# Optimization experiments

Hardware: AMD Instinct MI355X
Metric: run time of the kernel (lower is better)

## Reference

```python
import jax, jax.numpy as jnp
import numpy as np

D_MODEL = 512
N_LAYERS = 6
N_HEADS = 8
INNER = 2048
VOCAB = 2048
SEQ = 128
BATCH = 256
HEAD_DIM = D_MODEL // N_HEADS
EPS = 1e-5


def _pos_encoding(seq_len, d_model):
    pos = jnp.arange(seq_len, dtype=jnp.float32)[:, None]          # [S,1]
    i = jnp.arange(d_model // 2, dtype=jnp.float32)[None, :]       # [1,d/2]
    theta = pos / jnp.power(10000.0, 2.0 * i / d_model)            # [S,d/2]
    # interleave sin at even indices, cos at odd indices
    return jnp.stack([jnp.sin(theta), jnp.cos(theta)], axis=-1).reshape(seq_len, d_model)


def _layer_norm_2d(x):
    # F.layer_norm(x, (N, dims)): normalize over last TWO dims, no affine
    m = jnp.mean(x, axis=(1, 2), keepdims=True)
    v = jnp.mean(jnp.square(x - m), axis=(1, 2), keepdims=True)
    return (x - m) / jnp.sqrt(v + EPS)


def setup_inputs() -> dict:
    key = jax.random.key(0)
    ks = jax.random.split(key, 12)
    s = 0.02
    x = jax.random.randint(ks[0], (BATCH, SEQ), 0, VOCAB)
    emb = jax.random.normal(ks[1], (VOCAB, D_MODEL), jnp.float32) * s
    Wq = jax.random.normal(ks[2], (N_LAYERS, N_HEADS, D_MODEL, HEAD_DIM), jnp.float32) * s
    bq = jax.random.normal(ks[3], (N_LAYERS, N_HEADS, HEAD_DIM), jnp.float32) * s
    Wk = jax.random.normal(ks[4], (N_LAYERS, N_HEADS, D_MODEL, HEAD_DIM), jnp.float32) * s
    bk = jax.random.normal(ks[5], (N_LAYERS, N_HEADS, HEAD_DIM), jnp.float32) * s
    Wv = jax.random.normal(ks[6], (N_LAYERS, N_HEADS, D_MODEL, HEAD_DIM), jnp.float32) * s
    bv = jax.random.normal(ks[7], (N_LAYERS, N_HEADS, HEAD_DIM), jnp.float32) * s
    W1 = jax.random.normal(ks[8], (N_LAYERS, D_MODEL, INNER), jnp.float32) * s
    b1 = jax.random.normal(ks[9], (N_LAYERS, INNER), jnp.float32) * s
    W2 = jax.random.normal(ks[10], (N_LAYERS, INNER, D_MODEL), jnp.float32) * s
    b2 = jax.random.normal(ks[11], (N_LAYERS, D_MODEL), jnp.float32) * s
    return {"x": x, "emb": emb, "Wq": Wq, "bq": bq, "Wk": Wk, "bk": bk,
            "Wv": Wv, "bv": bv, "W1": W1, "b1": b1, "W2": W2, "b2": b2}


def reference(x, emb, Wq, bq, Wk, bk, Wv, bv, W1, b1, W2, b2):
    B, S = x.shape
    pe = _pos_encoding(SEQ, D_MODEL)
    h = emb[x] + pe[None, :, :]                                     # [B,S,D]
    scale = HEAD_DIM ** -0.5
    for l in range(N_LAYERS):
        q = jnp.einsum('bsd,hde->bhse', h, Wq[l]) + bq[l][None, :, None, :]
        k = jnp.einsum('bsd,hde->bhse', h, Wk[l]) + bk[l][None, :, None, :]
        v = jnp.einsum('bsd,hde->bhse', h, Wv[l]) + bv[l][None, :, None, :]
        scores = jnp.einsum('bhse,bhte->bhst', q, k) * scale        # no softmax!
        attn = jnp.einsum('bhst,bhte->bhse', scores, v)             # [B,H,S,E]
        attn = jnp.transpose(attn, (0, 2, 1, 3)).reshape(B, S, D_MODEL)
        h = _layer_norm_2d(h + attn)
        ff = jax.nn.relu(h @ W1[l] + b1[l]) @ W2[l] + b2[l]
        h = _layer_norm_2d(h + ff)
    return h
```

## Files before the change

kernel.cpp:

```cpp
#include <hip/hip_runtime.h>
#include <stdint.h>

#define NLAYERS 6
#define DMODEL  512
#define NHEADS  8
#define HDIM    64
#define INNER   2048
#define SEQ     128
#define BATCH   256
#define NTOK    (BATCH*SEQ)

typedef __attribute__((ext_vector_type(4))) float f32x4;
typedef __attribute__((ext_vector_type(8))) _Float16 hfrag;

typedef const __attribute__((address_space(1))) void* gas1p;
typedef __attribute__((address_space(3))) void* las3p;

__device__ __forceinline__ void load_lds16(const void* g, void* l) {
  __builtin_amdgcn_global_load_lds((gas1p)(uintptr_t)g, (las3p)(uint32_t)(uintptr_t)l, 16, 0, 0);
}

__device__ __forceinline__ ushort f2h(float f) {
  return __builtin_bit_cast(ushort, (_Float16)f);
}
__device__ __forceinline__ float h2f(ushort u) {
  return (float)__builtin_bit_cast(_Float16, u);
}

__device__ __forceinline__ f32x4 mfma16(hfrag a, hfrag b, f32x4 c) {
  return __builtin_amdgcn_mfma_f32_16x16x32_f16(a, b, c, 0, 0, 0);
}


__global__ void prep_qkv(const float* __restrict__ Wq, const float* __restrict__ Wk,
                         const float* __restrict__ Wv, const float* __restrict__ bq,
                         const float* __restrict__ bk, const float* __restrict__ bv,
                         ushort* __restrict__ Wt, float* __restrict__ biasq) {
  int idx = blockIdx.x*256 + threadIdx.x;
  if (idx >= NLAYERS*1536*512) return;
  const int k = idx & 511;
  const int n = (idx >> 9) % 1536;
  const int l = idx / (1536*512);
  const int which = n >> 9, hh = (n >> 6) & 7, e = n & 63;
  const float* W = (which == 0) ? Wq : ((which == 1) ? Wk : Wv);
  Wt[idx] = f2h(W[(((size_t)l*NHEADS + hh)*DMODEL + k)*HDIM + e]);
  if (k == 0) {
    const float* bb = (which == 0) ? bq : ((which == 1) ? bk : bv);
    biasq[l*1536 + n] = bb[((size_t)l*NHEADS + hh)*HDIM + e];
  }
}

__global__ void prep_w1(const float* __restrict__ W1, ushort* __restrict__ W1t) {
  int idx = blockIdx.x*256 + threadIdx.x;
  if (idx >= NLAYERS*INNER*512) return;
  const int k = idx & 511;
  const int n = (idx >> 9) % INNER;
  const int l = idx / (INNER*512);
  W1t[idx] = f2h(W1[((size_t)l*DMODEL + k)*INNER + n]);
}

__global__ void prep_w2(const float* __restrict__ W2, ushort* __restrict__ W2t) {
  int idx = blockIdx.x*256 + threadIdx.x;
  if (idx >= NLAYERS*512*INNER) return;
  const int k = idx & 2047;
  const int n = (idx >> 11) & 511;
  const int l = idx / (512*INNER);
  W2t[idx] = f2h(W2[((size_t)l*INNER + k)*DMODEL + n]);
}


__global__ void embed_kernel(const int* __restrict__ x, const float* __restrict__ emb,
                             ushort* __restrict__ hb) {
  const int t = blockIdx.x;
  const int i = threadIdx.x;
  const int s = t & (SEQ-1);
  const int tok = x[t];
  const float freq = expf(-(float)i * (9.210340371976184f / 256.0f));
  const float th = (float)s * freq;
  const float sn = sinf(th), cs = cosf(th);
  const size_t base = (size_t)t*DMODEL;
  const float v0 = emb[(size_t)tok*DMODEL + 2*i]     + sn;
  const float v1 = emb[(size_t)tok*DMODEL + 2*i + 1] + cs;
  *(uint*)(hb + base + 2*i) = (uint)f2h(v0) | ((uint)f2h(v1) << 16);
}


template<int K, int EPI>
__global__ __launch_bounds__(256, 2) void gemm_t(
    const ushort* __restrict__ A, const ushort* __restrict__ Bt,
    const float* __restrict__ bias, ushort* __restrict__ outb,
    const int ldc, const int nbn) {
  __shared__ __align__(16) char lds[73728];
  constexpr int NKT = K / 32;
  const int t = threadIdx.x;
  const int lane = t & 63, wc = t >> 6;
  const int cpx = (int)gridDim.x >> 3;
  const int wg  = ((int)blockIdx.x & 7) * cpx + ((int)blockIdx.x >> 3);
  const int bm = wg / nbn, bn = wg % nbn;

  const int fr = lane & 15;
  const int cxor = (((lane >> 4) ^ ((fr >> 1) & 3)) << 4);

  float bias_r[4];
  #pragma unroll
  for (int n = 0; n < 4; ++n) bias_r[n] = bias[bn*256 + wc*64 + n*16 + fr];
  asm volatile("" : "+v"(bias_r[0]), "+v"(bias_r[1]), "+v"(bias_r[2]), "+v"(bias_r[3]));

  const int srow = t >> 2;
  const int scc  = (t & 3) ^ ((t >> 3) & 3);
  const ushort* aSrc = A  + ((size_t)bm*128 + srow)*K + scc*8;
  const ushort* bSrc = Bt + ((size_t)bn*256 + srow)*K + scc*8;

  auto stage_t = [&](int j, int slot) {
    char* dst = lds + slot*24576 + t*16;
    const ushort* as = aSrc + j*32;
    load_lds16(as,                  dst);
    load_lds16(as + (size_t)64*K,   dst + 4096);
    const ushort* bs = bSrc + j*32;
    #pragma unroll
    for (int i = 0; i < 4; ++i)
      load_lds16(bs + (size_t)(i*64)*K, dst + 8192 + i*4096);
  };

  f32x4 acc[8][4] = {};

  stage_t(0, 0); stage_t(1, 1);
  asm volatile("s_waitcnt vmcnt(6)" ::: "memory");
  __builtin_amdgcn_s_barrier();

  int rs = 0, ss = 2;
  #pragma unroll 1
  for (int kt = 0; kt < NKT; ++kt) {
    const char* sl = lds + rs*24576;
    hfrag a[8], b[4];
    #pragma unroll
    for (int m = 0; m < 8; ++m)
      a[m] = *(const hfrag*)(sl + (m*16 + fr)*64 + cxor);
    #pragma unroll
    for (int n = 0; n < 4; ++n)
      b[n] = *(const hfrag*)(sl + 8192 + (wc*64 + n*16 + fr)*64 + cxor);
    if (kt + 2 < NKT) stage_t(kt + 2, ss);
    __builtin_amdgcn_s_setprio(1);
    #pragma unroll
    for (int m = 0; m < 8; ++m)
      #pragma unroll
      for (int n = 0; n < 4; ++n)
        acc[m][n] = mfma16(a[m], b[n], acc[m][n]);
    __builtin_amdgcn_s_setprio(0);
    if (kt + 2 < NKT) {
      asm volatile("s_waitcnt vmcnt(6)" ::: "memory");
    } else if (kt + 2 == NKT) {
      asm volatile("s_waitcnt vmcnt(0)" ::: "memory");
    }
    if (kt + 1 < NKT) __builtin_amdgcn_s_barrier();
    rs = (rs == 2) ? 0 : rs + 1;
    ss = (ss == 2) ? 0 : ss + 1;
  }

  #pragma unroll
  for (int m = 0; m < 8; ++m) {
    __syncthreads();
    #pragma unroll
    for (int n = 0; n < 4; ++n) {
      const int cc16 = wc*4 + n;
      #pragma unroll
      for (int r4 = 0; r4 < 4; ++r4) {
        const int row = ((lane >> 4) << 2) + r4;
        float v = acc[m][n][r4] + bias_r[n];
        if constexpr (EPI == 1) v = fmaxf(v, 0.0f);
        *(ushort*)(lds + row*512 + ((cc16 ^ (row >> 2)) << 5) + fr*2) = f2h(v);
      }
    }
    __syncthreads();
    const int er = t >> 4;
    ushort* gp = outb + (size_t)(bm*128 + m*16 + er)*ldc + bn*256;
    #pragma unroll
    for (int p = 0; p < 2; ++p) {
      const int cj = (t & 15) + p*16;
      const uint4 v = *(const uint4*)(lds + er*512 + (((cj >> 1) ^ (er >> 2)) << 5) + ((cj & 1) << 4));
      *(uint4*)(gp + cj*8) = v;
    }
  }
}


__global__ __launch_bounds__(256) void attn_kernel(
    const ushort* __restrict__ qkv, ushort* __restrict__ outb) {
  __shared__ __align__(16) ushort wbuf[4][8192];
  const int tid = threadIdx.x;
  const int w = tid >> 6, lane = tid & 63;
  const int bh = blockIdx.x*4 + w;
  const int b = bh >> 3, h = bh & 7;
  const ushort* tokbase = qkv + (size_t)b*SEQ*1536;
  ushort* lds = &wbuf[w][0];
  ushort* kch = lds;
  ushort* vch = lds + 2048;

  f32x4 acc1[4][4] = {};
  #pragma unroll 1
  for (int sb = 0; sb < 4; ++sb) {
    const int s0 = sb*32;
    const int sr = lane >> 1;
    #pragma unroll
    for (int i = 0; i < 4; ++i) {
      const int cc  = i*2 + (lane & 1);
      const int ccs = cc ^ (sr & 7);
      const ushort* g = tokbase + (size_t)(s0+sr)*1536 + h*64 + cc*8;
      *(uint4*)(kch + sr*64 + ccs*8) = *(const uint4*)(g + 512);
      *(uint4*)(vch + sr*64 + ccs*8) = *(const uint4*)(g + 1024);
    }
    hfrag ak[4], av[4];
    #pragma unroll
    for (int m = 0; m < 4; ++m) {
      const int e1 = m*16 + (lane & 15);
      const int ccb = e1 >> 3, el = e1 & 7;
      #pragma unroll
      for (int j = 0; j < 8; ++j) {
        const int s = (lane >> 4)*8 + j;
        ak[m][j] = __builtin_bit_cast(_Float16, kch[s*64 + ((ccb ^ (s & 7))*8) + el]);
        av[m][j] = __builtin_bit_cast(_Float16, vch[s*64 + ((ccb ^ (s & 7))*8) + el]);
      }
    }
    #pragma unroll
    for (int m = 0; m < 4; ++m)
      #pragma unroll
      for (int n = 0; n < 4; ++n)
        acc1[m][n] = mfma16(ak[m], av[n], acc1[m][n]);
  }

  ushort* tv = lds;
  #pragma unroll
  for (int m = 0; m < 4; ++m)
    #pragma unroll
    for (int n = 0; n < 4; ++n)
      #pragma unroll
      for (int r4 = 0; r4 < 4; ++r4) {
        const int e1 = m*16 + (lane >> 4)*4 + r4;
        const int e2 = n*16 + (lane & 15);
        tv[e2*72 + e1] = f2h(acc1[m][n][r4] * 0.125f);
      }

  f32x4 acc2[8][4] = {};
  #pragma unroll
  for (int eb = 0; eb < 2; ++eb) {
    const int e1b = eb*32 + (lane >> 4)*8;
    hfrag aq[8], bk2[4];
    #pragma unroll
    for (int m = 0; m < 8; ++m) {
      const int s = m*16 + (lane & 15);
      aq[m] = *(const hfrag*)(tokbase + (size_t)s*1536 + h*64 + e1b);
    }
    #pragma unroll
    for (int n = 0; n < 4; ++n) {
      const int e2 = n*16 + (lane & 15);
      bk2[n] = *(const hfrag*)(tv + e2*72 + e1b);
    }
    #pragma unroll
    for (int m = 0; m < 8; ++m)
      #pragma unroll
      for (int n = 0; n < 4; ++n)
        acc2[m][n] = mfma16(aq[m], bk2[n], acc2[m][n]);
  }

  const int fr = lane & 15;
  char* sb8 = (char*)lds;
  #pragma unroll
  for (int m = 0; m < 8; ++m)
    #pragma unroll
    for (int n = 0; n < 4; ++n)
      #pragma unroll
      for (int r4 = 0; r4 < 4; ++r4) {
        const int s = m*16 + ((lane >> 4) << 2) + r4;
        *(ushort*)(sb8 + s*128 + ((n ^ ((s >> 2) & 3)) << 5) + fr*2) = f2h(acc2[m][n][r4]);
      }
  ushort* ob = outb + ((size_t)b*SEQ)*DMODEL + h*64;
  #pragma unroll
  for (int rr = 0; rr < 16; ++rr) {
    const int r = rr*8 + (lane >> 3);
    const int cj = lane & 7;
    const uint4 v = *(const uint4*)(sb8 + r*128 + (((cj >> 1) ^ ((r >> 2) & 3)) << 5) + ((cj & 1) << 4));
    *(uint4*)(ob + (size_t)r*DMODEL + cj*8) = v;
  }
}


template<bool FINAL>
__global__ __launch_bounds__(1024) void resid_ln(
    const ushort* __restrict__ delta, ushort* __restrict__ hb, float* __restrict__ hf) {
  const int b = blockIdx.x;
  const size_t base = (size_t)b * (SEQ*DMODEL);
  uint4 cache[8];
  float s = 0.f, q = 0.f;
  #pragma unroll
  for (int j = 0; j < 8; ++j) {
    const size_t idx = base + (size_t)j*8192 + threadIdx.x*8;
    const uint4 hv = *(const uint4*)(hb + idx);
    const uint4 dv = *(const uint4*)(delta + idx);
    uint4 cv;
    #pragma unroll
    for (int c = 0; c < 4; ++c) {
      const uint hu = (&hv.x)[c], du = (&dv.x)[c];
      const float v0 = h2f((ushort)(hu & 0xffffu)) + h2f((ushort)(du & 0xffffu));
      const float v1 = h2f((ushort)(hu >> 16))     + h2f((ushort)(du >> 16));
      s += v0 + v1; q += v0*v0 + v1*v1;
      (&cv.x)[c] = (uint)f2h(v0) | ((uint)f2h(v1) << 16);
    }
    cache[j] = cv;
  }
  #pragma unroll
  for (int off = 32; off > 0; off >>= 1) {
    s += __shfl_down(s, off);
    q += __shfl_down(q, off);
  }
  __shared__ float ws_[16], wq_[16];
  __shared__ float stat[2];
  const int w = threadIdx.x >> 6, lane = threadIdx.x & 63;
  if (lane == 0) { ws_[w] = s; wq_[w] = q; }
  __syncthreads();
  if (threadIdx.x == 0) {
    float S = 0.f, Q = 0.f;
    #pragma unroll
    for (int i2 = 0; i2 < 16; ++i2) { S += ws_[i2]; Q += wq_[i2]; }
    const float mean = S * (1.0f/65536.0f);
    const float var  = Q * (1.0f/65536.0f) - mean*mean;
    stat[0] = mean; stat[1] = rsqrtf(var + 1e-5f);
  }
  __syncthreads();
  const float mean = stat[0], rstd = stat[1];
  #pragma unroll
  for (int j = 0; j < 8; ++j) {
    const size_t idx = base + (size_t)j*8192 + threadIdx.x*8;
    const uint4 cv = cache[j];
    if constexpr (FINAL) {
      #pragma unroll
      for (int c = 0; c < 4; ++c) {
        const uint u = (&cv.x)[c];
        const float o0 = (h2f((ushort)(u & 0xffffu)) - mean) * rstd;
        const float o1 = (h2f((ushort)(u >> 16))     - mean) * rstd;
        *(float2*)(hf + idx + c*2) = make_float2(o0, o1);
      }
    } else {
      uint4 ov;
      #pragma unroll
      for (int c = 0; c < 4; ++c) {
        const uint u = (&cv.x)[c];
        const float o0 = (h2f((ushort)(u & 0xffffu)) - mean) * rstd;
        const float o1 = (h2f((ushort)(u >> 16))     - mean) * rstd;
        (&ov.x)[c] = (uint)f2h(o0) | ((uint)f2h(o1) << 16);
      }
      *(uint4*)(hb + idx) = ov;
    }
  }
}


extern "C" void kernel_launch(void* const* d_in, const int* in_sizes, int n_in,
                              void* d_out, int out_size, void* d_ws, size_t ws_size,
                              hipStream_t stream) {
  const int*   x   = (const int*)d_in[0];
  const float* emb = (const float*)d_in[1];
  const float* Wq  = (const float*)d_in[2];
  const float* bq  = (const float*)d_in[3];
  const float* Wk  = (const float*)d_in[4];
  const float* bk  = (const float*)d_in[5];
  const float* Wv  = (const float*)d_in[6];
  const float* bv  = (const float*)d_in[7];
  const float* W1  = (const float*)d_in[8];
  const float* b1  = (const float*)d_in[9];
  const float* W2  = (const float*)d_in[10];
  const float* b2  = (const float*)d_in[11];
  float* h = (float*)d_out;

  char* p = (char*)d_ws;
  size_t off = 0;
  auto alloc = [&](size_t bytes) { char* r = p + off; off += (bytes + 255) & ~(size_t)255; return r; };
  ushort* Wqkv_t = (ushort*)alloc((size_t)NLAYERS*1536*512*2);
  ushort* W1t    = (ushort*)alloc((size_t)NLAYERS*INNER*512*2);
  ushort* W2t    = (ushort*)alloc((size_t)NLAYERS*512*INNER*2);
  float*  biasq  = (float*)alloc((size_t)NLAYERS*1536*4);
  ushort* hbf    = (ushort*)alloc((size_t)NTOK*512*2);
  ushort* big    = (ushort*)alloc((size_t)NTOK*2048*2);
  ushort* attnb  = (ushort*)alloc((size_t)NTOK*512*2);

  prep_qkv<<<(NLAYERS*1536*512 + 255)/256, 256, 0, stream>>>(Wq, Wk, Wv, bq, bk, bv, Wqkv_t, biasq);
  prep_w1<<<(NLAYERS*INNER*512 + 255)/256, 256, 0, stream>>>(W1, W1t);
  prep_w2<<<(NLAYERS*512*INNER + 255)/256, 256, 0, stream>>>(W2, W2t);
  embed_kernel<<<NTOK, 256, 0, stream>>>(x, emb, hbf);

  for (int l = 0; l < NLAYERS; ++l) {
    gemm_t<512,0><<<1536, 256, 0, stream>>>(
        hbf, Wqkv_t + (size_t)l*1536*512, biasq + (size_t)l*1536, big, 1536, 6);
    attn_kernel<<<BATCH*NHEADS/4, 256, 0, stream>>>(big, attnb);
    resid_ln<false><<<BATCH, 1024, 0, stream>>>(attnb, hbf, nullptr);
    gemm_t<512,1><<<2048, 256, 0, stream>>>(
        hbf, W1t + (size_t)l*INNER*512, b1 + (size_t)l*INNER, big, 2048, 8);
    gemm_t<2048,0><<<512, 256, 0, stream>>>(
        big, W2t + (size_t)l*512*INNER, b2 + (size_t)l*512, attnb, 512, 2);
    if (l == NLAYERS-1) {
      resid_ln<true><<<BATCH, 1024, 0, stream>>>(attnb, hbf, h);
    } else {
      resid_ln<false><<<BATCH, 1024, 0, stream>>>(attnb, hbf, nullptr);
    }
  }
}
```

Measured before the change: 1.750 ms.

## Enlarge GEMM tile to 256x256 with 8 waves and split-phase staging

New measurement: 1.764 ms. About the same (+0.8%).

```diff
diff --git a/kernel.cpp b/kernel.cpp
--- a/kernel.cpp
+++ b/kernel.cpp
@@ -86,14 +86,15 @@
 
 
 template<int K, int EPI>
-__global__ __launch_bounds__(256, 2) void gemm_t(
+__global__ __launch_bounds__(512, 2) void gemm_p(
     const ushort* __restrict__ A, const ushort* __restrict__ Bt,
     const float* __restrict__ bias, ushort* __restrict__ outb,
     const int ldc, const int nbn) {
-  __shared__ __align__(16) char lds[73728];
+  __shared__ __align__(16) char lds[98304];
   constexpr int NKT = K / 32;
   const int t = threadIdx.x;
-  const int lane = t & 63, wc = t >> 6;
+  const int lane = t & 63, w = t >> 6;
+  const int wr = w >> 2, wcn = w & 3;
   const int cpx = (int)gridDim.x >> 3;
   const int wg  = ((int)blockIdx.x & 7) * cpx + ((int)blockIdx.x >> 3);
   const int bm = wg / nbn, bn = wg % nbn;
@@ -103,52 +104,69 @@
 
   float bias_r[4];
   #pragma unroll
-  for (int n = 0; n < 4; ++n) bias_r[n] = bias[bn*256 + wc*64 + n*16 + fr];
+  for (int n = 0; n < 4; ++n) bias_r[n] = bias[bn*256 + wcn*64 + n*16 + fr];
   asm volatile("" : "+v"(bias_r[0]), "+v"(bias_r[1]), "+v"(bias_r[2]), "+v"(bias_r[3]));
 
   const int srow = t >> 2;
   const int scc  = (t & 3) ^ ((t >> 3) & 3);
-  const ushort* aSrc = A  + ((size_t)bm*128 + srow)*K + scc*8;
+  const ushort* aSrc = A  + ((size_t)bm*256 + srow)*K + scc*8;
   const ushort* bSrc = Bt + ((size_t)bn*256 + srow)*K + scc*8;
 
-  auto stage_t = [&](int j, int slot) {
-    char* dst = lds + slot*24576 + t*16;
+  auto stageA = [&](int j, int slot) {
+    char* dst = lds + slot*32768 + t*16;
     const ushort* as = aSrc + j*32;
-    load_lds16(as,                  dst);
-    load_lds16(as + (size_t)64*K,   dst + 4096);
+    load_lds16(as,                 dst);
+    load_lds16(as + (size_t)128*K, dst + 8192);
+  };
+  auto stageB = [&](int j, int slot) {
+    char* dst = lds + slot*32768 + 16384 + t*16;
     const ushort* bs = bSrc + j*32;
-    #pragma unroll
-    for (int i = 0; i < 4; ++i)
-      load_lds16(bs + (size_t)(i*64)*K, dst + 8192 + i*4096);
+    load_lds16(bs,                 dst);
+    load_lds16(bs + (size_t)128*K, dst + 8192);
   };
 
   f32x4 acc[8][4] = {};
 
-  stage_t(0, 0); stage_t(1, 1);
-  asm volatile("s_waitcnt vmcnt(6)" ::: "memory");
+  stageA(0, 0); stageB(0, 0); stageA(1, 1); stageB(1, 1);
+  asm volatile("s_waitcnt vmcnt(4)" ::: "memory");
   __builtin_amdgcn_s_barrier();
 
   int rs = 0, ss = 2;
   #pragma unroll 1
   for (int kt = 0; kt < NKT; ++kt) {
-    const char* sl = lds + rs*24576;
-    hfrag a[8], b[4];
-    #pragma unroll
-    for (int m = 0; m < 8; ++m)
-      a[m] = *(const hfrag*)(sl + (m*16 + fr)*64 + cxor);
+    const char* sl = lds + rs*32768;
+    hfrag a0[4], b0[4];
+    #pragma unroll
+    for (int m = 0; m < 4; ++m)
+      a0[m] = *(const hfrag*)(sl + (wr*128 + m*16 + fr)*64 + cxor);
     #pragma unroll
     for (int n = 0; n < 4; ++n)
-      b[n] = *(const hfrag*)(sl + 8192 + (wc*64 + n*16 + fr)*64 + cxor);
-    if (kt + 2 < NKT) stage_t(kt + 2, ss);
+      b0[n] = *(const hfrag*)(sl + 16384 + (wcn*64 + n*16 + fr)*64 + cxor);
+    if (kt + 2 < NKT) stageA(kt + 2, ss);
+    __builtin_amdgcn_s_barrier();
     __builtin_amdgcn_s_setprio(1);
     #pragma unroll
-    for (int m = 0; m < 8; ++m)
+    for (int m = 0; m < 4; ++m)
       #pragma unroll
       for (int n = 0; n < 4; ++n)
-        acc[m][n] = mfma16(a[m], b[n], acc[m][n]);
+        acc[m][n] = mfma16(a0[m], b0[n], acc[m][n]);
+    __builtin_amdgcn_s_setprio(0);
+    __builtin_amdgcn_s_barrier();
+    hfrag a1[4];
+    #pragma unroll
+    for (int m = 0; m < 4; ++m)
+      a1[m] = *(const hfrag*)(sl + (wr*128 + (m+4)*16 + fr)*64 + cxor);
+    if (kt + 2 < NKT) stageB(kt + 2, ss);
+    __builtin_amdgcn_s_barrier();
+    __builtin_amdgcn_s_setprio(1);
+    #pragma unroll
+    for (int m = 0; m < 4; ++m)
+      #pragma unroll
+      for (int n = 0; n < 4; ++n)
+        acc[m+4][n] = mfma16(a1[m], b0[n], acc[m+4][n]);
     __builtin_amdgcn_s_setprio(0);
     if (kt + 2 < NKT) {
-      asm volatile("s_waitcnt vmcnt(6)" ::: "memory");
+      asm volatile("s_waitcnt vmcnt(4)" ::: "memory");
     } else if (kt + 2 == NKT) {
       asm volatile("s_waitcnt vmcnt(0)" ::: "memory");
     }
@@ -162,22 +180,24 @@
     __syncthreads();
     #pragma unroll
     for (int n = 0; n < 4; ++n) {
-      const int cc16 = wc*4 + n;
       #pragma unroll
       for (int r4 = 0; r4 < 4; ++r4) {
-        const int row = ((lane >> 4) << 2) + r4;
+        const int sr32 = wr*16 + ((lane >> 4) << 2) + r4;
+        const int cc   = wcn*8 + n*2 + (fr >> 3);
+        const int ccs  = cc ^ (((sr32 >> 2) ^ sr32) & 3);
         float v = acc[m][n][r4] + bias_r[n];
         if constexpr (EPI == 1) v = fmaxf(v, 0.0f);
-        *(ushort*)(lds + row*512 + ((cc16 ^ (row >> 2)) << 5) + fr*2) = f2h(v);
+        *(ushort*)(lds + sr32*512 + ccs*16 + (fr & 7)*2) = f2h(v);
       }
     }
     __syncthreads();
-    const int er = t >> 4;
-    ushort* gp = outb + (size_t)(bm*128 + m*16 + er)*ldc + bn*256;
+    const int lr = t >> 4;
+    const int grow = bm*256 + (lr >> 4)*128 + m*16 + (lr & 15);
+    ushort* gp = outb + (size_t)grow*ldc + bn*256;
     #pragma unroll
     for (int p = 0; p < 2; ++p) {
       const int cj = (t & 15) + p*16;
-      const uint4 v = *(const uint4*)(lds + er*512 + (((cj >> 1) ^ (er >> 2)) << 5) + ((cj & 1) << 4));
+      const uint4 v = *(const uint4*)(lds + lr*512 + (cj ^ (((lr >> 2) ^ lr) & 3))*16);
       *(uint4*)(gp + cj*8) = v;
     }
   }
@@ -388,13 +408,13 @@
   embed_kernel<<<NTOK, 256, 0, stream>>>(x, emb, hbf);
 
   for (int l = 0; l < NLAYERS; ++l) {
-    gemm_t<512,0><<<1536, 256, 0, stream>>>(
+    gemm_p<512,0><<<768, 512, 0, stream>>>(
         hbf, Wqkv_t + (size_t)l*1536*512, biasq + (size_t)l*1536, big, 1536, 6);
     attn_kernel<<<BATCH*NHEADS/4, 256, 0, stream>>>(big, attnb);
     resid_ln<false><<<BATCH, 1024, 0, stream>>>(attnb, hbf, nullptr);
-    gemm_t<512,1><<<2048, 256, 0, stream>>>(
+    gemm_p<512,1><<<1024, 512, 0, stream>>>(
         hbf, W1t + (size_t)l*INNER*512, b1 + (size_t)l*INNER, big, 2048, 8);
-    gemm_t<2048,0><<<512, 256, 0, stream>>>(
+    gemm_p<2048,0><<<256, 512, 0, stream>>>(
         big, W2t + (size_t)l*512*INNER, b2 + (size_t)l*512, attnb, 512, 2);
     if (l == NLAYERS-1) {
       resid_ln<true><<<BATCH, 1024, 0, stream>>>(attnb, hbf, h);
```

## Rewrite GEMM with 256x256 tiles, 32x32 MFMA and double-buffered K=64 stages

Applied to the files above, without the earlier changes.

Result: slower. 2.180 ms (+24.5%).

```diff
diff --git a/kernel.cpp b/kernel.cpp
--- a/kernel.cpp
+++ b/kernel.cpp
@@ -10,8 +10,9 @@
 #define BATCH   256
 #define NTOK    (BATCH*SEQ)
 
-typedef __attribute__((ext_vector_type(4))) float f32x4;
-typedef __attribute__((ext_vector_type(8))) _Float16 hfrag;
+typedef __attribute__((ext_vector_type(4)))  float f32x4;
+typedef __attribute__((ext_vector_type(16))) float f32x16;
+typedef __attribute__((ext_vector_type(8)))  _Float16 hfrag;
 
 typedef const __attribute__((address_space(1))) void* gas1p;
 typedef __attribute__((address_space(3))) void* las3p;
@@ -29,6 +30,9 @@
 
 __device__ __forceinline__ f32x4 mfma16(hfrag a, hfrag b, f32x4 c) {
   return __builtin_amdgcn_mfma_f32_16x16x32_f16(a, b, c, 0, 0, 0);
+}
+__device__ __forceinline__ f32x16 mfma32(hfrag a, hfrag b, f32x16 c) {
+  return __builtin_amdgcn_mfma_f32_32x32x16_f16(a, b, c, 0, 0, 0);
 }
 
 
@@ -86,100 +90,92 @@
 
 
 template<int K, int EPI>
-__global__ __launch_bounds__(256, 2) void gemm_t(
+__global__ __launch_bounds__(256, 1) void gemm_w(
     const ushort* __restrict__ A, const ushort* __restrict__ Bt,
     const float* __restrict__ bias, ushort* __restrict__ outb,
     const int ldc, const int nbn) {
-  __shared__ __align__(16) char lds[73728];
-  constexpr int NKT = K / 32;
+  __shared__ __align__(16) char lds[131072];
+  constexpr int NKT = K / 64;
   const int t = threadIdx.x;
-  const int lane = t & 63, wc = t >> 6;
+  const int lane = t & 63, w = t >> 6;
+  const int wr = w >> 1, wc = w & 1;
   const int cpx = (int)gridDim.x >> 3;
   const int wg  = ((int)blockIdx.x & 7) * cpx + ((int)blockIdx.x >> 3);
   const int bm = wg / nbn, bn = wg % nbn;
 
-  const int fr = lane & 15;
-  const int cxor = (((lane >> 4) ^ ((fr >> 1) & 3)) << 4);
-
   float bias_r[4];
   #pragma unroll
-  for (int n = 0; n < 4; ++n) bias_r[n] = bias[bn*256 + wc*64 + n*16 + fr];
+  for (int n = 0; n < 4; ++n) bias_r[n] = bias[bn*256 + wc*128 + n*32 + (lane & 31)];
   asm volatile("" : "+v"(bias_r[0]), "+v"(bias_r[1]), "+v"(bias_r[2]), "+v"(bias_r[3]));
 
-  const int srow = t >> 2;
-  const int scc  = (t & 3) ^ ((t >> 3) & 3);
-  const ushort* aSrc = A  + ((size_t)bm*128 + srow)*K + scc*8;
-  const ushort* bSrc = Bt + ((size_t)bn*256 + srow)*K + scc*8;
-
-  auto stage_t = [&](int j, int slot) {
-    char* dst = lds + slot*24576 + t*16;
-    const ushort* as = aSrc + j*32;
-    load_lds16(as,                  dst);
-    load_lds16(as + (size_t)64*K,   dst + 4096);
-    const ushort* bs = bSrc + j*32;
-    #pragma unroll
-    for (int i = 0; i < 4; ++i)
-      load_lds16(bs + (size_t)(i*64)*K, dst + 8192 + i*4096);
+  const int srow = t >> 3;
+  const int gcc  = (t & 7) ^ (srow & 7);
+  const ushort* aSrc = A  + ((size_t)bm*256 + srow)*K + gcc*8;
+  const ushort* bSrc = Bt + ((size_t)bn*256 + srow)*K + gcc*8;
+
+  auto stage = [&](int j, int slot) {
+    char* da = lds + slot*65536 + t*16;
+    const ushort* as = aSrc + j*64;
+    const ushort* bs = bSrc + j*64;
+    #pragma unroll
+    for (int i = 0; i < 8; ++i) {
+      load_lds16(as + (size_t)(i*32)*K, da + i*4096);
+      load_lds16(bs + (size_t)(i*32)*K, da + 32768 + i*4096);
+    }
   };
 
-  f32x4 acc[8][4] = {};
-
-  stage_t(0, 0); stage_t(1, 1);
-  asm volatile("s_waitcnt vmcnt(6)" ::: "memory");
+  f32x16 acc[4][4] = {};
+
+  stage(0, 0);
+  asm volatile("s_waitcnt vmcnt(0)" ::: "memory");
   __builtin_amdgcn_s_barrier();
 
-  int rs = 0, ss = 2;
   #pragma unroll 1
   for (int kt = 0; kt < NKT; ++kt) {
-    const char* sl = lds + rs*24576;
-    hfrag a[8], b[4];
-    #pragma unroll
-    for (int m = 0; m < 8; ++m)
-      a[m] = *(const hfrag*)(sl + (m*16 + fr)*64 + cxor);
+    if (kt + 1 < NKT) stage(kt + 1, (kt + 1) & 1);
+    const char* sl = lds + (kt & 1)*65536;
+    const char* sa = sl + (size_t)(wr*128 + (lane & 31))*128;
+    const char* sb = sl + 32768 + (size_t)(wc*128 + (lane & 31))*128;
+    #pragma unroll
+    for (int kk = 0; kk < 4; ++kk) {
+      const int slotx = ((kk*2 + (lane >> 5)) ^ (lane & 7)) * 16;
+      hfrag a[4], b[4];
+      #pragma unroll
+      for (int m = 0; m < 4; ++m) a[m] = *(const hfrag*)(sa + m*4096 + slotx);
+      #pragma unroll
+      for (int n = 0; n < 4; ++n) b[n] = *(const hfrag*)(sb + n*4096 + slotx);
+      #pragma unroll
+      for (int m = 0; m < 4; ++m)
+        #pragma unroll
+        for (int n = 0; n < 4; ++n)
+          acc[m][n] = mfma32(a[m], b[n], acc[m][n]);
+    }
+    if (kt + 1 < NKT) {
+      asm volatile("s_waitcnt vmcnt(0)" ::: "memory");
+    }
+    __builtin_amdgcn_s_barrier();
+  }
+
+  __syncthreads();
+  #pragma unroll
+  for (int m = 0; m < 4; ++m)
     #pragma unroll
     for (int n = 0; n < 4; ++n)
-      b[n] = *(const hfrag*)(sl + 8192 + (wc*64 + n*16 + fr)*64 + cxor);
-    if (kt + 2 < NKT) stage_t(kt + 2, ss);
-    __builtin_amdgcn_s_setprio(1);
-    #pragma unroll
-    for (int m = 0; m < 8; ++m)
-      #pragma unroll
-      for (int n = 0; n < 4; ++n)
-        acc[m][n] = mfma16(a[m], b[n], acc[m][n]);
-    __builtin_amdgcn_s_setprio(0);
-    if (kt + 2 < NKT) {
-      asm volatile("s_waitcnt vmcnt(6)" ::: "memory");
-    } else if (kt + 2 == NKT) {
-      asm volatile("s_waitcnt vmcnt(0)" ::: "memory");
-    }
-    if (kt + 1 < NKT) __builtin_amdgcn_s_barrier();
-    rs = (rs == 2) ? 0 : rs + 1;
-    ss = (ss == 2) ? 0 : ss + 1;
-  }
-
-  #pragma unroll
-  for (int m = 0; m < 8; ++m) {
-    __syncthreads();
-    #pragma unroll
-    for (int n = 0; n < 4; ++n) {
-      const int cc16 = wc*4 + n;
-      #pragma unroll
-      for (int r4 = 0; r4 < 4; ++r4) {
-        const int row = ((lane >> 4) << 2) + r4;
-        float v = acc[m][n][r4] + bias_r[n];
+      #pragma unroll
+      for (int r = 0; r < 16; ++r) {
+        const int row = wr*128 + m*32 + (r & 3) + 8*(r >> 2) + 4*(lane >> 5);
+        const int col = wc*128 + n*32 + (lane & 31);
+        float v = acc[m][n][r] + bias_r[n];
         if constexpr (EPI == 1) v = fmaxf(v, 0.0f);
-        *(ushort*)(lds + row*512 + ((cc16 ^ (row >> 2)) << 5) + fr*2) = f2h(v);
-      }
-    }
-    __syncthreads();
-    const int er = t >> 4;
-    ushort* gp = outb + (size_t)(bm*128 + m*16 + er)*ldc + bn*256;
-    #pragma unroll
-    for (int p = 0; p < 2; ++p) {
-      const int cj = (t & 15) + p*16;
-      const uint4 v = *(const uint4*)(lds + er*512 + (((cj >> 1) ^ (er >> 2)) << 5) + ((cj & 1) << 4));
-      *(uint4*)(gp + cj*8) = v;
-    }
+        *(ushort*)(lds + row*512 + ((col*2) ^ ((row & 7) << 4))) = f2h(v);
+      }
+  __syncthreads();
+  #pragma unroll
+  for (int p = 0; p < 32; ++p) {
+    const int lr = p*8 + (t >> 5);
+    const int ck = t & 31;
+    const uint4 v = *(const uint4*)(lds + lr*512 + ((ck*16) ^ ((lr & 7) << 4)));
+    *(uint4*)(outb + (size_t)(bm*256 + lr)*ldc + bn*256 + ck*8) = v;
   }
 }
 
@@ -388,13 +384,13 @@
   embed_kernel<<<NTOK, 256, 0, stream>>>(x, emb, hbf);
 
   for (int l = 0; l < NLAYERS; ++l) {
-    gemm_t<512,0><<<1536, 256, 0, stream>>>(
+    gemm_w<512,0><<<768, 256, 0, stream>>>(
         hbf, Wqkv_t + (size_t)l*1536*512, biasq + (size_t)l*1536, big, 1536, 6);
     attn_kernel<<<BATCH*NHEADS/4, 256, 0, stream>>>(big, attnb);
     resid_ln<false><<<BATCH, 1024, 0, stream>>>(attnb, hbf, nullptr);
-    gemm_t<512,1><<<2048, 256, 0, stream>>>(
+    gemm_w<512,1><<<1024, 256, 0, stream>>>(
         hbf, W1t + (size_t)l*INNER*512, b1 + (size_t)l*INNER, big, 2048, 8);
-    gemm_t<2048,0><<<512, 256, 0, stream>>>(
+    gemm_w<2048,0><<<256, 256, 0, stream>>>(
         big, W2t + (size_t)l*512*INNER, b2 + (size_t)l*512, attnb, 512, 2);
     if (l == NLAYERS-1) {
       resid_ln<true><<<BATCH, 1024, 0, stream>>>(attnb, hbf, h);
```

## Fuse residual layernorm into attention and FFN2 GEMM kernels

Applied to the files above, without the earlier changes.

Result: faster. 1.664 ms (-4.9%).

```diff
diff --git a/kernel.cpp b/kernel.cpp
--- a/kernel.cpp
+++ b/kernel.cpp
@@ -184,17 +184,18 @@
 }
 
 
-__global__ __launch_bounds__(256) void attn_kernel(
-    const ushort* __restrict__ qkv, ushort* __restrict__ outb) {
-  __shared__ __align__(16) ushort wbuf[4][8192];
-  const int tid = threadIdx.x;
-  const int w = tid >> 6, lane = tid & 63;
-  const int bh = blockIdx.x*4 + w;
-  const int b = bh >> 3, h = bh & 7;
+__global__ __launch_bounds__(512, 1) void attn_ln(
+    const ushort* __restrict__ qkv, ushort* __restrict__ hb) {
+  __shared__ __align__(16) char lds[131072];
+  __shared__ float red_[8], redq_[8], stat_[2];
+  const int t = threadIdx.x;
+  const int w = t >> 6, lane = t & 63;
+  const int b = blockIdx.x, h = w;
+  const int fr = lane & 15;
   const ushort* tokbase = qkv + (size_t)b*SEQ*1536;
-  ushort* lds = &wbuf[w][0];
-  ushort* kch = lds;
-  ushort* vch = lds + 2048;
+  ushort* wl  = (ushort*)(lds + w*16384);
+  ushort* kch = wl;
+  ushort* vch = wl + 2048;
 
   f32x4 acc1[4][4] = {};
   #pragma unroll 1
@@ -228,7 +229,7 @@
         acc1[m][n] = mfma16(ak[m], av[n], acc1[m][n]);
   }
 
-  ushort* tv = lds;
+  ushort* tv = wl;
   #pragma unroll
   for (int m = 0; m < 4; ++m)
     #pragma unroll
@@ -262,93 +263,227 @@
         acc2[m][n] = mfma16(aq[m], bk2[n], acc2[m][n]);
   }
 
+  __syncthreads();
+  #pragma unroll
+  for (int m = 0; m < 8; ++m)
+    #pragma unroll
+    for (int n = 0; n < 4; ++n)
+      #pragma unroll
+      for (int r4 = 0; r4 < 4; ++r4) {
+        const int row = m*16 + ((lane >> 4) << 2) + r4;
+        const int ch  = (w*4 + n) ^ ((row >> 2) & 3) ^ (w >> 1);
+        *(ushort*)(lds + row*1024 + ch*32 + fr*2) = f2h(acc2[m][n][r4]);
+      }
+  __syncthreads();
+
+  const int r = t >> 2, qd = t & 3;
+  const ushort* hrow = hb + ((size_t)b*SEQ + r)*DMODEL + qd*128;
+  uint4 vc[16];
+  float s = 0.f, q2 = 0.f;
+  #pragma unroll
+  for (int j = 0; j < 8; ++j) {
+    const int ch = (qd*8 + j) ^ ((r >> 2) & 3) ^ qd;
+    const uint4 d0 = *(const uint4*)(lds + r*1024 + ch*32);
+    const uint4 d1 = *(const uint4*)(lds + r*1024 + ch*32 + 16);
+    const uint4 h0 = *(const uint4*)(hrow + j*16);
+    const uint4 h1 = *(const uint4*)(hrow + j*16 + 8);
+    uint4 v0, v1;
+    #pragma unroll
+    for (int c = 0; c < 4; ++c) {
+      float a0 = h2f((ushort)((&h0.x)[c] & 0xffffu)) + h2f((ushort)((&d0.x)[c] & 0xffffu));
+      float a1 = h2f((ushort)((&h0.x)[c] >> 16))     + h2f((ushort)((&d0.x)[c] >> 16));
+      float b0 = h2f((ushort)((&h1.x)[c] & 0xffffu)) + h2f((ushort)((&d1.x)[c] & 0xffffu));
+      float b1 = h2f((ushort)((&h1.x)[c] >> 16))     + h2f((ushort)((&d1.x)[c] >> 16));
+      s += a0 + a1 + b0 + b1;
+      q2 += a0*a0 + a1*a1 + b0*b0 + b1*b1;
+      (&v0.x)[c] = (uint)f2h(a0) | ((uint)f2h(a1) << 16);
+      (&v1.x)[c] = (uint)f2h(b0) | ((uint)f2h(b1) << 16);
+    }
+    vc[2*j] = v0; vc[2*j+1] = v1;
+  }
+  #pragma unroll
+  for (int off = 32; off > 0; off >>= 1) {
+    s  += __shfl_down(s, off);
+    q2 += __shfl_down(q2, off);
+  }
+  if (lane == 0) { red_[w] = s; redq_[w] = q2; }
+  __syncthreads();
+  if (t == 0) {
+    float S = 0.f, Q = 0.f;
+    #pragma unroll
+    for (int i = 0; i < 8; ++i) { S += red_[i]; Q += redq_[i]; }
+    const float mean = S * (1.0f/65536.0f);
+    stat_[0] = mean;
+    stat_[1] = rsqrtf(Q * (1.0f/65536.0f) - mean*mean + 1e-5f);
+  }
+  __syncthreads();
+  const float mean = stat_[0], rstd = stat_[1];
+  ushort* orow = hb + ((size_t)b*SEQ + r)*DMODEL + qd*128;
+  #pragma unroll
+  for (int j = 0; j < 16; ++j) {
+    const uint4 u = vc[j];
+    uint4 o;
+    #pragma unroll
+    for (int c = 0; c < 4; ++c) {
+      const float o0 = (h2f((ushort)((&u.x)[c] & 0xffffu)) - mean) * rstd;
+      const float o1 = (h2f((ushort)((&u.x)[c] >> 16))     - mean) * rstd;
+      (&o.x)[c] = (uint)f2h(o0) | ((uint)f2h(o1) << 16);
+    }
+    *(uint4*)(orow + j*8) = o;
+  }
+}
+
+
+template<bool FINAL>
+__global__ __launch_bounds__(512, 1) void gemm_f(
+    const ushort* __restrict__ A, const ushort* __restrict__ Bt,
+    const float* __restrict__ bias, ushort* __restrict__ hb, float* __restrict__ hf) {
+  __shared__ __align__(16) char lds[131072];
+  __shared__ float red_[8], redq_[8], stat_[2];
+  constexpr int K = 2048, NKT = 64;
+  const int t = threadIdx.x;
+  const int lane = t & 63, w = t >> 6;
+  const int bm = blockIdx.x;
   const int fr = lane & 15;
-  char* sb8 = (char*)lds;
+  const int cxor = (((lane >> 4) ^ ((fr >> 1) & 3)) << 4);
+
+  float bias_r[4];
+  #pragma unroll
+  for (int n = 0; n < 4; ++n) bias_r[n] = bias[w*64 + n*16 + fr];
+  asm volatile("" : "+v"(bias_r[0]), "+v"(bias_r[1]), "+v"(bias_r[2]), "+v"(bias_r[3]));
+
+  const int srow = t >> 2;
+  const int scc  = (t & 3) ^ ((t >> 3) & 3);
+  const ushort* aSrc = A  + ((size_t)bm*128 + srow)*K + scc*8;
+  const ushort* bSrc = Bt + (size_t)srow*K + scc*8;
+
+  auto stage = [&](int j, int slot) {
+    char* dst = lds + slot*40960 + t*16;
+    load_lds16(aSrc + j*32, dst);
+    #pragma unroll
+    for (int i = 0; i < 4; ++i)
+      load_lds16(bSrc + (size_t)(i*128)*K + j*32, dst + 8192 + i*8192);
+  };
+
+  f32x4 acc[8][4] = {};
+
+  stage(0, 0); stage(1, 1);
+  asm volatile("s_waitcnt vmcnt(5)" ::: "memory");
+  __builtin_amdgcn_s_barrier();
+
+  int rs = 0, ss = 2;
+  #pragma unroll 1
+  for (int kt = 0; kt < NKT; ++kt) {
+    const char* sl = lds + rs*40960;
+    hfrag a[8], b[4];
+    #pragma unroll
+    for (int m = 0; m < 8; ++m)
+      a[m] = *(const hfrag*)(sl + (m*16 + fr)*64 + cxor);
+    #pragma unroll
+    for (int n = 0; n < 4; ++n)
+      b[n] = *(const hfrag*)(sl + 8192 + (w*64 + n*16 + fr)*64 + cxor);
+    if (kt + 2 < NKT) stage(kt + 2, ss);
+    __builtin_amdgcn_s_setprio(1);
+    #pragma unroll
+    for (int m = 0; m < 8; ++m)
+      #pragma unroll
+      for (int n = 0; n < 4; ++n)
+        acc[m][n] = mfma16(a[m], b[n], acc[m][n]);
+    __builtin_amdgcn_s_setprio(0);
+    if (kt + 2 < NKT) {
+      asm volatile("s_waitcnt vmcnt(5)" ::: "memory");
+    } else if (kt + 2 == NKT) {
+      asm volatile("s_waitcnt vmcnt(0)" ::: "memory");
+    }
+    if (kt + 1 < NKT) __builtin_amdgcn_s_barrier();
+    rs = (rs == 2) ? 0 : rs + 1;
+    ss = (ss == 2) ? 0 : ss + 1;
+  }
+
+  __syncthreads();
   #pragma unroll
   for (int m = 0; m < 8; ++m)
     #pragma unroll
     for (int n = 0; n < 4; ++n)
       #pragma unroll
       for (int r4 = 0; r4 < 4; ++r4) {
-        const int s = m*16 + ((lane >> 4) << 2) + r4;
-        *(ushort*)(sb8 + s*128 + ((n ^ ((s >> 2) & 3)) << 5) + fr*2) = f2h(acc2[m][n][r4]);
-      }
-  ushort* ob = outb + ((size_t)b*SEQ)*DMODEL + h*64;
-  #pragma unroll
-  for (int rr = 0; rr < 16; ++rr) {
-    const int r = rr*8 + (lane >> 3);
-    const int cj = lane & 7;
-    const uint4 v = *(const uint4*)(sb8 + r*128 + (((cj >> 1) ^ ((r >> 2) & 3)) << 5) + ((cj & 1) << 4));
-    *(uint4*)(ob + (size_t)r*DMODEL + cj*8) = v;
-  }
-}
-
-
-template<bool FINAL>
-__global__ __launch_bounds__(1024) void resid_ln(
-    const ushort* __restrict__ delta, ushort* __restrict__ hb, float* __restrict__ hf) {
-  const int b = blockIdx.x;
-  const size_t base = (size_t)b * (SEQ*DMODEL);
-  uint4 cache[8];
-  float s = 0.f, q = 0.f;
+        const int row = m*16 + ((lane >> 4) << 2) + r4;
+        const int ch  = (w*4 + n) ^ ((row >> 2) & 3) ^ (w >> 1);
+        *(ushort*)(lds + row*1024 + ch*32 + fr*2) = f2h(acc[m][n][r4] + bias_r[n]);
+      }
+  __syncthreads();
+
+  const int r = t >> 2, qd = t & 3;
+  const ushort* hrow = hb + ((size_t)bm*SEQ + r)*DMODEL + qd*128;
+  uint4 vc[16];
+  float s = 0.f, q2 = 0.f;
   #pragma unroll
   for (int j = 0; j < 8; ++j) {
-    const size_t idx = base + (size_t)j*8192 + threadIdx.x*8;
-    const uint4 hv = *(const uint4*)(hb + idx);
-    const uint4 dv = *(const uint4*)(delta + idx);
-    uint4 cv;
+    const int ch = (qd*8 + j) ^ ((r >> 2) & 3) ^ qd;
+    const uint4 d0 = *(const uint4*)(lds + r*1024 + ch*32);
+    const uint4 d1 = *(const uint4*)(lds + r*1024 + ch*32 + 16);
+    const uint4 h0 = *(const uint4*)(hrow + j*16);
+    const uint4 h1 = *(const uint4*)(hrow + j*16 + 8);
+    uint4 v0, v1;
     #pragma unroll
     for (int c = 0; c < 4; ++c) {
-      const uint hu = (&hv.x)[c], du = (&dv.x)[c];
-      const float v0 = h2f((ushort)(hu & 0xffffu)) + h2f((ushort)(du & 0xffffu));
-      const float v1 = h2f((ushort)(hu >> 16))     + h2f((ushort)(du >> 16));
-      s += v0 + v1; q += v0*v0 + v1*v1;
-      (&cv.x)[c] = (uint)f2h(v0) | ((uint)f2h(v1) << 16);
-    }
-    cache[j] = cv;
+      float a0 = h2f((ushort)((&h0.x)[c] & 0xffffu)) + h2f((ushort)((&d0.x)[c] & 0xffffu));
+      float a1 = h2f((ushort)((&h0.x)[c] >> 16))     + h2f((ushort)((&d0.x)[c] >> 16));
+      float b0 = h2f((ushort)((&h1.x)[c] & 0xffffu)) + h2f((ushort)((&d1.x)[c] & 0xffffu));
+      float b1 = h2f((ushort)((&h1.x)[c] >> 16))     + h2f((ushort)((&d1.x)[c] >> 16));
+      s += a0 + a1 + b0 + b1;
+      q2 += a0*a0 + a1*a1 + b0*b0 + b1*b1;
+      (&v0.x)[c] = (uint)f2h(a0) | ((uint)f2h(a1) << 16);
+      (&v1.x)[c] = (uint)f2h(b0) | ((uint)f2h(b1) << 16);
+    }
+    vc[2*j] = v0; vc[2*j+1] = v1;
   }
   #pragma unroll
   for (int off = 32; off > 0; off >>= 1) {
-    s += __shfl_down(s, off);
-    q += __shfl_down(q, off);
-  }
-  __shared__ float ws_[16], wq_[16];
-  __shared__ float stat[2];
-  const int w = threadIdx.x >> 6, lane = threadIdx.x & 63;
-  if (lane == 0) { ws_[w] = s; wq_[w] = q; }
-  __syncthreads();
-  if (threadIdx.x == 0) {
+    s  += __shfl_down(s, off);
+    q2 += __shfl_down(q2, off);
+  }
+  if (lane == 0) { red_[w] = s; redq_[w] = q2; }
+  __syncthreads();
+  if (t == 0) {
     float S = 0.f, Q = 0.f;
     #pragma unroll
-    for (int i2 = 0; i2 < 16; ++i2) { S += ws_[i2]; Q += wq_[i2]; }
+    for (int i = 0; i < 8; ++i) { S += red_[i]; Q += redq_[i]; }
     const float mean = S * (1.0f/65536.0f);
-    const float var  = Q * (1.0f/65536.0f) - mean*mean;
-    stat[0] = mean; stat[1] = rsqrtf(var + 1e-5f);
-  }
-  __syncthreads();
-  const float mean = stat[0], rstd = stat[1];
-  #pragma unroll
-  for (int j = 0; j < 8; ++j) {
-    const size_t idx = base + (size_t)j*8192 + threadIdx.x*8;
-    const uint4 cv = cache[j];
-    if constexpr (FINAL) {
+    stat_[0] = mean;
+    stat_[1] = rsqrtf(Q * (1.0f/65536.0f) - mean*mean + 1e-5f);
+  }
+  __syncthreads();
+  const float mean = stat_[0], rstd = stat_[1];
+  if constexpr (FINAL) {
+    float* frow = hf + ((size_t)bm*SEQ + r)*DMODEL + qd*128;
+    #pragma unroll
+    for (int j = 0; j < 16; ++j) {
+      const uint4 u = vc[j];
+      f32x4 o0, o1;
+      #pragma unroll
+      for (int c = 0; c < 2; ++c) {
+        o0[2*c]   = (h2f((ushort)((&u.x)[c] & 0xffffu)) - mean) * rstd;
+        o0[2*c+1] = (h2f((ushort)((&u.x)[c] >> 16))     - mean) * rstd;
+        o1[2*c]   = (h2f((ushort)((&u.x)[c+2] & 0xffffu)) - mean) * rstd;
+        o1[2*c+1] = (h2f((ushort)((&u.x)[c+2] >> 16))     - mean) * rstd;
+      }
+      *(f32x4*)(frow + j*8)     = o0;
+      *(f32x4*)(frow + j*8 + 4) = o1;
+    }
+  } else {
+    ushort* orow = hb + ((size_t)bm*SEQ + r)*DMODEL + qd*128;
+    #pragma unroll
+    for (int j = 0; j < 16; ++j) {
+      const uint4 u = vc[j];
+      uint4 o;
       #pragma unroll
       for (int c = 0; c < 4; ++c) {
-        const uint u = (&cv.x)[c];
-        const float o0 = (h2f((ushort)(u & 0xffffu)) - mean) * rstd;
-        const float o1 = (h2f((ushort)(u >> 16))     - mean) * rstd;
-        *(float2*)(hf + idx + c*2) = make_float2(o0, o1);
-      }
-    } else {
-      uint4 ov;
-      #pragma unroll
-      for (int c = 0; c < 4; ++c) {
-        const uint u = (&cv.x)[c];
-        const float o0 = (h2f((ushort)(u & 0xffffu)) - mean) * rstd;
-        const float o1 = (h2f((ushort)(u >> 16))     - mean) * rstd;
-        (&ov.x)[c] = (uint)f2h(o0) | ((uint)f2h(o1) << 16);
-      }
-      *(uint4*)(hb + idx) = ov;
+        const float o0 = (h2f((ushort)((&u.x)[c] & 0xffffu)) - mean) * rstd;
+        const float o1 = (h2f((ushort)((&u.x)[c] >> 16))     - mean) * rstd;
+        (&o.x)[c] = (uint)f2h(o0) | ((uint)f2h(o1) << 16);
+      }
+      *(uint4*)(orow + j*8) = o;
     }
   }
 }
@@ -380,7 +515,6 @@
   float*  biasq  = (float*)alloc((size_t)NLAYERS*1536*4);
   ushort* hbf    = (ushort*)alloc((size_t)NTOK*512*2);
   ushort* big    = (ushort*)alloc((size_t)NTOK*2048*2);
-  ushort* attnb  = (ushort*)alloc((size_t)NTOK*512*2);
 
   prep_qkv<<<(NLAYERS*1536*512 + 255)/256, 256, 0, stream>>>(Wq, Wk, Wv, bq, bk, bv, Wqkv_t, biasq);
   prep_w1<<<(NLAYERS*INNER*512 + 255)/256, 256, 0, stream>>>(W1, W1t);
@@ -390,16 +524,15 @@
   for (int l = 0; l < NLAYERS; ++l) {
     gemm_t<512,0><<<1536, 256, 0, stream>>>(
         hbf, Wqkv_t + (size_t)l*1536*512, biasq + (size_t)l*1536, big, 1536, 6);
-    attn_kernel<<<BATCH*NHEADS/4, 256, 0, stream>>>(big, attnb);
-    resid_ln<false><<<BATCH, 1024, 0, stream>>>(attnb, hbf, nullptr);
+    attn_ln<<<BATCH, 512, 0, stream>>>(big, hbf);
     gemm_t<512,1><<<2048, 256, 0, stream>>>(
         hbf, W1t + (size_t)l*INNER*512, b1 + (size_t)l*INNER, big, 2048, 8);
-    gemm_t<2048,0><<<512, 256, 0, stream>>>(
-        big, W2t + (size_t)l*512*INNER, b2 + (size_t)l*512, attnb, 512, 2);
     if (l == NLAYERS-1) {
-      resid_ln<true><<<BATCH, 1024, 0, stream>>>(attnb, hbf, h);
+      gemm_f<true><<<BATCH, 512, 0, stream>>>(
+          big, W2t + (size_t)l*512*INNER, b2 + (size_t)l*512, hbf, h);
     } else {
-      resid_ln<false><<<BATCH, 1024, 0, stream>>>(attnb, hbf, nullptr);
-    }
-  }
-}
+      gemm_f<false><<<BATCH, 512, 0, stream>>>(
+          big, W2t + (size_t)l*512*INNER, b2 + (size_t)l*512, hbf, nullptr);
+    }
+  }
+}
```
